# Performance work log

Hardware: AMD Instinct MI355X
Metric: run time of the kernel (lower is better)

Reference implementation:

```python
import jax, jax.numpy as jnp
import numpy as np

EPS = 1e-06

def rmsnorm(x, w):
    x32 = x.astype(jnp.float32)
    var = jnp.mean(x32 * x32, axis=-1, keepdims=True)
    return w * (x32 * jax.lax.rsqrt(var + EPS)).astype(x.dtype)

def setup_inputs() -> dict:
    B, T, C = 16, 256, 16
    token_dim, text_dim = 1024, 512
    key = jax.random.key(0)
    ks = jax.random.split(key, 8)
    token_embeds = jax.random.normal(ks[0], (B, T, token_dim), dtype=jnp.float32)
    char_embeds = jax.random.normal(ks[1], (B, T, C, text_dim), dtype=jnp.float32)
    filler_embed = jax.random.normal(ks[2], (text_dim,), dtype=jnp.float32)
    mask = jax.random.randint(ks[3], (B, T, C), 0, 2).astype(bool)
    mask = mask.at[0].set(True)  # force max valid count == T*C (static output shape)
    token_ids_mask = jnp.ones((B, T), dtype=bool)
    # xavier-uniform-ish weights
    def xav(k, fan_out, fan_in, gain=1.0):
        lim = gain * np.sqrt(6.0 / (fan_in + fan_out))
        return jax.random.uniform(k, (fan_out, fan_in), jnp.float32, -lim, lim)
    W_down = xav(ks[4], text_dim, token_dim)
    W_proj = xav(ks[5], 3, text_dim, gain=0.2)
    W_fusion = xav(ks[6], text_dim, text_dim)
    w_pre = jnp.ones((token_dim,), jnp.float32)
    w_tok = jnp.ones((text_dim,), jnp.float32)
    w_char = jnp.ones((text_dim,), jnp.float32)
    return {"token_embeds": token_embeds, "token_ids_mask": token_ids_mask,
            "char_embeds": char_embeds, "char_ids_mask": mask,
            "filler_embed": filler_embed, "w_pre": w_pre, "w_tok": w_tok,
            "w_char": w_char, "W_down": W_down, "W_proj": W_proj,
            "W_fusion": W_fusion, "max_valid_chars": T * C}

def reference(token_embeds, token_ids_mask, char_embeds, char_ids_mask,
              filler_embed, w_pre, w_tok, w_char, W_down, W_proj, W_fusion,
              max_valid_chars):
    B, T, C, d = char_embeds.shape
    MV = int(max_valid_chars)
    tok = rmsnorm(token_embeds, w_pre)                       # [B,T,token_dim]
    feats = rmsnorm(jnp.einsum('btk,dk->btd', tok, W_down), w_tok)  # [B,T,d]
    params = jnp.einsum('btd,pd->btp', jax.nn.silu(feats), W_proj)  # [B,T,3]
    scale = params[..., 0][:, :, None, None]                 # [B,T,1,1]
    shift = params[..., 1][:, :, None, None]
    gate = jax.nn.sigmoid(params[..., 2][:, :, None, None])
    cn = rmsnorm(char_embeds, w_char)                        # [B,T,C,d]
    fused = jnp.einsum('btcd,ed->btce', jax.nn.silu(cn * (1.0 + scale) + shift), W_fusion)
    fused = gate * fused + (1.0 - gate) * cn                 # [B,T,C,d]
    flat = fused.reshape(B, T * C, d)
    m = char_ids_mask.reshape(B, T * C).astype(jnp.int32)
    pos = jnp.cumsum(m, axis=1) - 1                          # dest within row
    offs = jnp.arange(B, dtype=jnp.int32)[:, None] * MV
    idx = jnp.where(m > 0, offs + pos, B * MV)               # invalid -> dump slot
    buf = jnp.broadcast_to(filler_embed, (B * MV + 1, d))
    buf = buf.at[idx.reshape(-1)].set(flat.reshape(-1, d))
    return buf[: B * MV].reshape(B, MV, d)
```

## Files before the change

kernel.cpp:

```cpp
#include <hip/hip_runtime.h>
#include <cstdint>
#include <cstddef>

#define EPS 1e-6f

typedef short bf16x8 __attribute__((ext_vector_type(8)));
typedef float f32x4  __attribute__((ext_vector_type(4)));

__device__ __forceinline__ short f2bf(float x) {
    uint32_t u = __builtin_bit_cast(uint32_t, x);
    return (short)((u + 0x7FFFu + ((u >> 16) & 1u)) >> 16);
}

__global__ __launch_bounds__(256) void k_scan(const void* __restrict__ maskp,
                                              int* __restrict__ v_list,
                                              int* __restrict__ counts) {
    __shared__ int sc[256];
    __shared__ int mode_s;
    const int tid = threadIdx.x;
    const int b = blockIdx.x;
    const uint32_t* mi = (const uint32_t*)maskp;
    const uint8_t* mb = (const uint8_t*)maskp;

    if (tid == 0) mode_s = 0;
    __syncthreads();
    int bad = 0;
    for (int k = tid; k < 1024; k += 256) bad |= (mi[k] > 1u) ? 1 : 0;
    if (bad) mode_s = 1;
    __syncthreads();
    const int byte_mode = mode_s;

    int base = 0;
    for (int chunk = 0; chunk < 16; ++chunk) {
        const int i = chunk * 256 + tid;
        int m;
        if (byte_mode) m = mb[(b << 12) + i] ? 1 : 0;
        else           m = mi[(b << 12) + i] ? 1 : 0;
        sc[tid] = m;
        __syncthreads();
        for (int off = 1; off < 256; off <<= 1) {
            int v = sc[tid];
            int a = (tid >= off) ? sc[tid - off] : 0;
            __syncthreads();
            sc[tid] = v + a;
            __syncthreads();
        }
        const int incl = sc[tid];
        const int tot = sc[255];
        if (m) v_list[(b << 12) + base + incl - 1] = i;
        base += tot;
        __syncthreads();
    }
    if (tid == 0) counts[b] = base;
}

__global__ __launch_bounds__(256) void k_conv(const float* __restrict__ src,
                                              short* __restrict__ dst, int n4) {
    const int gid = blockIdx.x * 256 + threadIdx.x;
    if (gid >= n4) return;
    const float4 v = ((const float4*)src)[gid];
    short4 o;
    o.x = f2bf(v.x); o.y = f2bf(v.y); o.z = f2bf(v.z); o.w = f2bf(v.w);
    ((short4*)dst)[gid] = o;
}

__global__ __launch_bounds__(256) void k_tokprep(const float* __restrict__ tokens,
                                                 const float* __restrict__ w_pre,
                                                 short* __restrict__ tokbf) {
    const int tid = threadIdx.x, lane = tid & 63, wave = tid >> 6;
    const int row = blockIdx.x * 4 + wave;
    const float* xp = tokens + (size_t)row * 1024 + lane * 16;
    float4 x[4];
#pragma unroll
    for (int q = 0; q < 4; ++q) x[q] = *(const float4*)&xp[q * 4];
    float ss = 0.f;
#pragma unroll
    for (int q = 0; q < 4; ++q)
        ss += x[q].x * x[q].x + x[q].y * x[q].y + x[q].z * x[q].z + x[q].w * x[q].w;
#pragma unroll
    for (int off = 32; off > 0; off >>= 1) ss += __shfl_down(ss, off);
    ss = __shfl(ss, 0);
    const float r = rsqrtf(ss * (1.0f / 1024.0f) + EPS);
    const float* wp = w_pre + lane * 16;
    short* op = tokbf + (size_t)row * 1024 + lane * 16;
#pragma unroll
    for (int h = 0; h < 2; ++h) {
        bf16x8 o;
#pragma unroll
        for (int q = 0; q < 2; ++q) {
            const float4 wv = *(const float4*)&wp[h * 8 + q * 4];
            const float4 xv = x[h * 2 + q];
            o[q * 4 + 0] = f2bf(xv.x * wv.x * r);
            o[q * 4 + 1] = f2bf(xv.y * wv.y * r);
            o[q * 4 + 2] = f2bf(xv.z * wv.z * r);
            o[q * 4 + 3] = f2bf(xv.w * wv.w * r);
        }
        *(bf16x8*)&op[h * 8] = o;
    }
}

__global__ __launch_bounds__(256) void k_gemm_tok(const short* __restrict__ tokbf,
                                                  const short* __restrict__ Wdbf,
                                                  float* __restrict__ feats) {
    __shared__ short As[128 * 32];
    __shared__ short Bs[128 * 32];
    const int tid = threadIdx.x, lane = tid & 63, w = tid >> 6;
    const int mt = blockIdx.x >> 2, nt = blockIdx.x & 3;
    const int wm = w >> 1, wn = w & 1;
    const short* hA = tokbf + (size_t)mt * 128 * 1024;
    const short* wB = Wdbf + (size_t)nt * 128 * 1024;

    f32x4 acc[4][4];
#pragma unroll
    for (int mi = 0; mi < 4; ++mi)
#pragma unroll
        for (int ni = 0; ni < 4; ++ni) acc[mi][ni] = (f32x4)0.f;

    const int rA = lane & 15, q8 = (lane >> 4) * 8;
    for (int kk = 0; kk < 1024; kk += 32) {
#pragma unroll
        for (int q = 0; q < 2; ++q) {
            const int cid = (w * 2 + q) * 64 + lane;
            const int r = cid >> 2, kc = cid & 3;
            const size_t go = (size_t)r * 1024 + kk + kc * 8;
            __builtin_amdgcn_global_load_lds(
                (const __attribute__((address_space(1))) uint32_t*)(hA + go),
                (__attribute__((address_space(3))) uint32_t*)&As[(w * 2 + q) * 512], 16, 0, 0);
            __builtin_amdgcn_global_load_lds(
                (const __attribute__((address_space(1))) uint32_t*)(wB + go),
                (__attribute__((address_space(3))) uint32_t*)&Bs[(w * 2 + q) * 512], 16, 0, 0);
        }
        __syncthreads();
        bf16x8 af[4], bfr[4];
#pragma unroll
        for (int mi = 0; mi < 4; ++mi)
            af[mi] = *(const bf16x8*)&As[(wm * 64 + mi * 16 + rA) * 32 + q8];
#pragma unroll
        for (int ni = 0; ni < 4; ++ni)
            bfr[ni] = *(const bf16x8*)&Bs[(wn * 64 + ni * 16 + rA) * 32 + q8];
#pragma unroll
        for (int mi = 0; mi < 4; ++mi)
#pragma unroll
            for (int ni = 0; ni < 4; ++ni)
                acc[mi][ni] = __builtin_amdgcn_mfma_f32_16x16x32_bf16(af[mi], bfr[ni], acc[mi][ni], 0, 0, 0);
        __syncthreads();
    }
    const int rowb = mt * 128 + wm * 64 + (lane >> 4) * 4;
    const int colb = nt * 128 + wn * 64 + (lane & 15);
#pragma unroll
    for (int mi = 0; mi < 4; ++mi)
#pragma unroll
        for (int ni = 0; ni < 4; ++ni)
#pragma unroll
            for (int rg = 0; rg < 4; ++rg)
                feats[(size_t)(rowb + mi * 16 + rg) * 512 + colb + ni * 16] = acc[mi][ni][rg];
}

__global__ __launch_bounds__(64) void k_params(
    const float* __restrict__ feats_pre, const float* __restrict__ w_tok,
    const float* __restrict__ W_proj, float* __restrict__ params) {
    const int tk = blockIdx.x;
    const int lane = threadIdx.x;
    const int d0 = lane * 8;
    const float* fp = feats_pre + (size_t)tk * 512 + d0;
    const float4 f0 = *(const float4*)&fp[0];
    const float4 f1 = *(const float4*)&fp[4];
    float ss = f0.x * f0.x + f0.y * f0.y + f0.z * f0.z + f0.w * f0.w
             + f1.x * f1.x + f1.y * f1.y + f1.z * f1.z + f1.w * f1.w;
#pragma unroll
    for (int off = 32; off > 0; off >>= 1) ss += __shfl_down(ss, off);
    ss = __shfl(ss, 0);
    const float rms = rsqrtf(ss * (1.0f / 512.0f) + EPS);

    const float4 wt0 = *(const float4*)&w_tok[d0];
    const float4 wt1 = *(const float4*)&w_tok[d0 + 4];
    float fv[8] = {f0.x, f0.y, f0.z, f0.w, f1.x, f1.y, f1.z, f1.w};
    float wv[8] = {wt0.x, wt0.y, wt0.z, wt0.w, wt1.x, wt1.y, wt1.z, wt1.w};
    float s[8];
#pragma unroll
    for (int j = 0; j < 8; ++j) {
        const float v = fv[j] * wv[j] * rms;
        s[j] = v / (1.0f + expf(-v));
    }
    float p[3];
#pragma unroll
    for (int q = 0; q < 3; ++q) {
        const float* Wp = W_proj + (size_t)q * 512 + d0;
        const float4 a = *(const float4*)&Wp[0];
        const float4 c = *(const float4*)&Wp[4];
        p[q] = s[0] * a.x + s[1] * a.y + s[2] * a.z + s[3] * a.w
             + s[4] * c.x + s[5] * c.y + s[6] * c.z + s[7] * c.w;
#pragma unroll
        for (int off = 32; off > 0; off >>= 1) p[q] += __shfl_down(p[q], off);
    }
    if (lane == 0) {
        float* po = params + (size_t)tk * 4;
        po[0] = 1.0f + p[0];
        po[1] = p[1];
        po[2] = 1.0f / (1.0f + expf(-p[2]));
    }
}

__global__ __launch_bounds__(256) void k_prep(
    const float* __restrict__ chars, const float* __restrict__ w_char,
    const float* __restrict__ params, const int* __restrict__ v_list,
    const int* __restrict__ counts, short* __restrict__ hb,
    float* __restrict__ rms_l, float* __restrict__ g_l) {
    const int tid = threadIdx.x, lane = tid & 63, wave = tid >> 6;
    const int b = blockIdx.x >> 10;
    const int j = (blockIdx.x & 1023) * 4 + wave;
    const int cnt = counts[b];
    const int cpad = (cnt + 127) & ~127;
    if (j >= cpad) return;
    short* hrow = hb + ((size_t)(b << 12) + j) * 512 + lane * 8;
    if (j >= cnt) {
        *(bf16x8*)hrow = (bf16x8)0;
        return;
    }
    const int i = v_list[(b << 12) + j];
    const float* xp = chars + ((size_t)(b << 12) + i) * 512 + lane * 8;
    const float4 x0 = *(const float4*)&xp[0];
    const float4 x1 = *(const float4*)&xp[4];
    float ss = x0.x * x0.x + x0.y * x0.y + x0.z * x0.z + x0.w * x0.w
             + x1.x * x1.x + x1.y * x1.y + x1.z * x1.z + x1.w * x1.w;
#pragma unroll
    for (int off = 32; off > 0; off >>= 1) ss += __shfl_down(ss, off);
    ss = __shfl(ss, 0);
    const float rms = rsqrtf(ss * (1.0f / 512.0f) + EPS);
    const float* pp = params + (size_t)((b << 8) + (i >> 4)) * 4;
    const float s1 = pp[0], sh = pp[1], g = pp[2];
    const float4 w0 = *(const float4*)&w_char[lane * 8];
    const float4 w1 = *(const float4*)&w_char[lane * 8 + 4];
    float xv[8] = {x0.x, x0.y, x0.z, x0.w, x1.x, x1.y, x1.z, x1.w};
    float wv[8] = {w0.x, w0.y, w0.z, w0.w, w1.x, w1.y, w1.z, w1.w};
    bf16x8 o;
#pragma unroll
    for (int q = 0; q < 8; ++q) {
        const float cn = wv[q] * xv[q] * rms;
        const float a = cn * s1 + sh;
        o[q] = f2bf(a / (1.0f + expf(-a)));
    }
    *(bf16x8*)hrow = o;
    if (lane == 0) {
        rms_l[(b << 12) + j] = rms;
        g_l[(b << 12) + j] = g;
    }
}

__global__ __launch_bounds__(256) void k_fill(
    const float* __restrict__ filler, const int* __restrict__ counts,
    float* __restrict__ out) {
    const int gid = blockIdx.x * 256 + threadIdx.x;
    const size_t e4 = (size_t)gid * 4;
    const int slot = gid >> 7;
    const int b = slot >> 12;
    const int j = slot & 4095;
    if (j >= counts[b]) {
        const int e0 = (int)(e4 & 511);
        *(float4*)&out[e4] = *(const float4*)&filler[e0];
    }
}

__global__ __launch_bounds__(256) void k_gemm_fus(
    const short* __restrict__ hb, const short* __restrict__ Wbf,
    const float* __restrict__ chars, const float* __restrict__ w_char,
    const float* __restrict__ rms_l, const float* __restrict__ g_l,
    const int* __restrict__ v_list, const int* __restrict__ counts,
    float* __restrict__ out) {
    __shared__ short As[128 * 32];
    __shared__ short Bs[128 * 32];
    __shared__ float g_s[128], rms_s[128];
    __shared__ int idx_s[128];
    const int tid = threadIdx.x, lane = tid & 63, w = tid >> 6;
    const int b = blockIdx.x >> 7;
    const int mt = (blockIdx.x >> 2) & 31;
    const int nt = blockIdx.x & 3;
    const int cnt = counts[b];
    const int row0 = mt * 128;
    if (row0 >= cnt) return;
    const int wm = w >> 1, wn = w & 1;

    if (tid < 128) {
        const int j = row0 + tid;
        const bool valid = j < cnt;
        idx_s[tid] = valid ? v_list[(b << 12) + j] : 0;
        g_s[tid]   = valid ? g_l[(b << 12) + j] : 0.f;
        rms_s[tid] = valid ? rms_l[(b << 12) + j] : 0.f;
    }

    const short* hA = hb + ((size_t)(b << 12) + row0) * 512;
    const short* wB = Wbf + (size_t)nt * 128 * 512;

    f32x4 acc[4][4];
#pragma unroll
    for (int mi = 0; mi < 4; ++mi)
#pragma unroll
        for (int ni = 0; ni < 4; ++ni) acc[mi][ni] = (f32x4)0.f;

    const int rA = lane & 15, q8 = (lane >> 4) * 8;
    for (int kk = 0; kk < 512; kk += 32) {
#pragma unroll
        for (int q = 0; q < 2; ++q) {
            const int cid = (w * 2 + q) * 64 + lane;
            const int r = cid >> 2, kc = cid & 3;
            const size_t go = (size_t)r * 512 + kk + kc * 8;
            __builtin_amdgcn_global_load_lds(
                (const __attribute__((address_space(1))) uint32_t*)(hA + go),
                (__attribute__((address_space(3))) uint32_t*)&As[(w * 2 + q) * 512], 16, 0, 0);
            __builtin_amdgcn_global_load_lds(
                (const __attribute__((address_space(1))) uint32_t*)(wB + go),
                (__attribute__((address_space(3))) uint32_t*)&Bs[(w * 2 + q) * 512], 16, 0, 0);
        }
        __syncthreads();
        bf16x8 af[4], bfr[4];
#pragma unroll
        for (int mi = 0; mi < 4; ++mi)
            af[mi] = *(const bf16x8*)&As[(wm * 64 + mi * 16 + rA) * 32 + q8];
#pragma unroll
        for (int ni = 0; ni < 4; ++ni)
            bfr[ni] = *(const bf16x8*)&Bs[(wn * 64 + ni * 16 + rA) * 32 + q8];
#pragma unroll
        for (int mi = 0; mi < 4; ++mi)
#pragma unroll
            for (int ni = 0; ni < 4; ++ni)
                acc[mi][ni] = __builtin_amdgcn_mfma_f32_16x16x32_bf16(af[mi], bfr[ni], acc[mi][ni], 0, 0, 0);
        __syncthreads();
    }

    const int colb = nt * 128 + wn * 64 + (lane & 15);
    float wcv[4];
#pragma unroll
    for (int ni = 0; ni < 4; ++ni) wcv[ni] = w_char[colb + ni * 16];
#pragma unroll
    for (int mi = 0; mi < 4; ++mi) {
#pragma unroll
        for (int rg = 0; rg < 4; ++rg) {
            const int jl = wm * 64 + mi * 16 + (lane >> 4) * 4 + rg;
            const int j = row0 + jl;
            if (j < cnt) {
                const float g = g_s[jl], rm = rms_s[jl];
                const size_t xrow = ((size_t)(b << 12) + idx_s[jl]) * 512;
                const size_t orow = ((size_t)(b << 12) + j) * 512;
#pragma unroll
                for (int ni = 0; ni < 4; ++ni) {
                    const int col = colb + ni * 16;
                    const float x = chars[xrow + col];
                    const float cn = wcv[ni] * x * rm;
                    out[orow + col] = g * acc[mi][ni][rg] + (1.0f - g) * cn;
                }
            }
        }
    }
}

extern "C" void kernel_launch(void* const* d_in, const int* in_sizes, int n_in,
                              void* d_out, int out_size, void* d_ws, size_t ws_size,
                              hipStream_t stream) {
    const float* tokens = (const float*)d_in[0];
    const float* chars  = (const float*)d_in[2];
    const void*  cmask  = d_in[3];
    const float* filler = (const float*)d_in[4];
    const float* w_pre  = (const float*)d_in[5];
    const float* w_tok  = (const float*)d_in[6];
    const float* w_char = (const float*)d_in[7];
    const float* W_down = (const float*)d_in[8];
    const float* W_proj = (const float*)d_in[9];
    const float* W_fus  = (const float*)d_in[10];
    float* out = (float*)d_out;

    float* feats_pre = (float*)d_ws;
    float* params    = feats_pre + (size_t)4096 * 512;
    int*   counts    = (int*)(params + (size_t)4096 * 4);
    int*   v_list    = counts + 16;
    float* rms_l     = (float*)(v_list + 65536);
    float* g_l       = rms_l + 65536;
    short* Wbf       = (short*)(g_l + 65536);
    short* hb        = Wbf + (size_t)512 * 512;
    short* tokbf     = hb + (size_t)16 * 4096 * 512;
    short* Wdbf      = tokbf + (size_t)4096 * 1024;

    k_scan<<<16, 256, 0, stream>>>(cmask, v_list, counts);
    k_conv<<<256, 256, 0, stream>>>(W_fus, Wbf, 65536);
    k_conv<<<512, 256, 0, stream>>>(W_down, Wdbf, 131072);
    k_tokprep<<<1024, 256, 0, stream>>>(tokens, w_pre, tokbf);
    k_gemm_tok<<<128, 256, 0, stream>>>(tokbf, Wdbf, feats_pre);
    k_params<<<4096, 64, 0, stream>>>(feats_pre, w_tok, W_proj, params);
    k_prep<<<16384, 256, 0, stream>>>(chars, w_char, params, v_list, counts, hb, rms_l, g_l);
    k_fill<<<32768, 256, 0, stream>>>(filler, counts, out);
    k_gemm_fus<<<2048, 256, 0, stream>>>(hb, Wbf, chars, w_char, rms_l, g_l, v_list, counts, out);
}
```

Baseline: 370.0 us.

## Restructure scan, fuse weight converts, retile token GEMM, precompute bf16 residual epilogue

```diff
diff --git a/kernel.cpp b/kernel.cpp
--- a/kernel.cpp
+++ b/kernel.cpp
@@ -10,6 +10,10 @@
 __device__ __forceinline__ short f2bf(float x) {
     uint32_t u = __builtin_bit_cast(uint32_t, x);
     return (short)((u + 0x7FFFu + ((u >> 16) & 1u)) >> 16);
+}
+__device__ __forceinline__ float bf2f(short s) {
+    uint32_t u = ((uint32_t)(uint16_t)s) << 16;
+    return __builtin_bit_cast(float, u);
 }
 
 __global__ __launch_bounds__(256) void k_scan(const void* __restrict__ maskp,
@@ -20,7 +24,6 @@
     const int tid = threadIdx.x;
     const int b = blockIdx.x;
     const uint32_t* mi = (const uint32_t*)maskp;
-    const uint8_t* mb = (const uint8_t*)maskp;
 
     if (tid == 0) mode_s = 0;
     __syncthreads();
@@ -28,40 +31,53 @@
     for (int k = tid; k < 1024; k += 256) bad |= (mi[k] > 1u) ? 1 : 0;
     if (bad) mode_s = 1;
     __syncthreads();
-    const int byte_mode = mode_s;
-
-    int base = 0;
-    for (int chunk = 0; chunk < 16; ++chunk) {
-        const int i = chunk * 256 + tid;
-        int m;
-        if (byte_mode) m = mb[(b << 12) + i] ? 1 : 0;
-        else           m = mi[(b << 12) + i] ? 1 : 0;
-        sc[tid] = m;
-        __syncthreads();
-        for (int off = 1; off < 256; off <<= 1) {
-            int v = sc[tid];
-            int a = (tid >= off) ? sc[tid - off] : 0;
-            __syncthreads();
-            sc[tid] = v + a;
-            __syncthreads();
-        }
-        const int incl = sc[tid];
-        const int tot = sc[255];
-        if (m) v_list[(b << 12) + base + incl - 1] = i;
-        base += tot;
-        __syncthreads();
-    }
-    if (tid == 0) counts[b] = base;
-}
-
-__global__ __launch_bounds__(256) void k_conv(const float* __restrict__ src,
-                                              short* __restrict__ dst, int n4) {
+
+    int m[16];
+    if (mode_s) {
+        const uint4 v = *(const uint4*)((const uint8_t*)maskp + (b << 12) + tid * 16);
+        const uint32_t ws[4] = {v.x, v.y, v.z, v.w};
+#pragma unroll
+        for (int w4 = 0; w4 < 4; ++w4)
+#pragma unroll
+            for (int e = 0; e < 4; ++e)
+                m[w4 * 4 + e] = ((ws[w4] >> (8 * e)) & 0xffu) ? 1 : 0;
+    } else {
+        const uint32_t* p = mi + (b << 12) + tid * 16;
+#pragma unroll
+        for (int q = 0; q < 16; ++q) m[q] = p[q] ? 1 : 0;
+    }
+    int cl = 0;
+#pragma unroll
+    for (int q = 0; q < 16; ++q) cl += m[q];
+    sc[tid] = cl;
+    __syncthreads();
+    for (int off = 1; off < 256; off <<= 1) {
+        int v = sc[tid];
+        int a = (tid >= off) ? sc[tid - off] : 0;
+        __syncthreads();
+        sc[tid] = v + a;
+        __syncthreads();
+    }
+    int pos = sc[tid] - cl;
+#pragma unroll
+    for (int q = 0; q < 16; ++q) {
+        if (m[q]) v_list[(b << 12) + pos++] = tid * 16 + q;
+    }
+    if (tid == 255) counts[b] = sc[255];
+}
+
+__global__ __launch_bounds__(256) void k_conv2(
+    const float* __restrict__ s1, short* __restrict__ d1, int n1,
+    const float* __restrict__ s2, short* __restrict__ d2, int n2) {
     const int gid = blockIdx.x * 256 + threadIdx.x;
-    if (gid >= n4) return;
-    const float4 v = ((const float4*)src)[gid];
+    const float* src; short* dst; int idx;
+    if (gid < n1) { src = s1; dst = d1; idx = gid; }
+    else if (gid < n1 + n2) { src = s2; dst = d2; idx = gid - n1; }
+    else return;
+    const float4 v = ((const float4*)src)[idx];
     short4 o;
     o.x = f2bf(v.x); o.y = f2bf(v.y); o.z = f2bf(v.z); o.w = f2bf(v.w);
-    ((short4*)dst)[gid] = o;
+    ((short4*)dst)[idx] = o;
 }
 
 __global__ __launch_bounds__(256) void k_tokprep(const float* __restrict__ tokens,
@@ -103,18 +119,18 @@
                                                   const short* __restrict__ Wdbf,
                                                   float* __restrict__ feats) {
     __shared__ short As[128 * 32];
-    __shared__ short Bs[128 * 32];
+    __shared__ short Bs[64 * 32];
     const int tid = threadIdx.x, lane = tid & 63, w = tid >> 6;
-    const int mt = blockIdx.x >> 2, nt = blockIdx.x & 3;
+    const int mt = blockIdx.x >> 3, nt = blockIdx.x & 7;
     const int wm = w >> 1, wn = w & 1;
     const short* hA = tokbf + (size_t)mt * 128 * 1024;
-    const short* wB = Wdbf + (size_t)nt * 128 * 1024;
-
-    f32x4 acc[4][4];
+    const short* wB = Wdbf + (size_t)nt * 64 * 1024;
+
+    f32x4 acc[4][2];
 #pragma unroll
     for (int mi = 0; mi < 4; ++mi)
 #pragma unroll
-        for (int ni = 0; ni < 4; ++ni) acc[mi][ni] = (f32x4)0.f;
+        for (int ni = 0; ni < 2; ++ni) acc[mi][ni] = (f32x4)0.f;
 
     const int rA = lane & 15, q8 = (lane >> 4) * 8;
     for (int kk = 0; kk < 1024; kk += 32) {
@@ -122,35 +138,38 @@
         for (int q = 0; q < 2; ++q) {
             const int cid = (w * 2 + q) * 64 + lane;
             const int r = cid >> 2, kc = cid & 3;
-            const size_t go = (size_t)r * 1024 + kk + kc * 8;
             __builtin_amdgcn_global_load_lds(
-                (const __attribute__((address_space(1))) uint32_t*)(hA + go),
+                (const __attribute__((address_space(1))) uint32_t*)(hA + (size_t)r * 1024 + kk + kc * 8),
                 (__attribute__((address_space(3))) uint32_t*)&As[(w * 2 + q) * 512], 16, 0, 0);
+        }
+        {
+            const int cid = tid;
+            const int r = cid >> 2, kc = cid & 3;
             __builtin_amdgcn_global_load_lds(
-                (const __attribute__((address_space(1))) uint32_t*)(wB + go),
-                (__attribute__((address_space(3))) uint32_t*)&Bs[(w * 2 + q) * 512], 16, 0, 0);
+                (const __attribute__((address_space(1))) uint32_t*)(wB + (size_t)r * 1024 + kk + kc * 8),
+                (__attribute__((address_space(3))) uint32_t*)&Bs[w * 512], 16, 0, 0);
         }
         __syncthreads();
-        bf16x8 af[4], bfr[4];
+        bf16x8 af[4], bfr[2];
 #pragma unroll
         for (int mi = 0; mi < 4; ++mi)
             af[mi] = *(const bf16x8*)&As[(wm * 64 + mi * 16 + rA) * 32 + q8];
 #pragma unroll
-        for (int ni = 0; ni < 4; ++ni)
-            bfr[ni] = *(const bf16x8*)&Bs[(wn * 64 + ni * 16 + rA) * 32 + q8];
+        for (int ni = 0; ni < 2; ++ni)
+            bfr[ni] = *(const bf16x8*)&Bs[(wn * 32 + ni * 16 + rA) * 32 + q8];
 #pragma unroll
         for (int mi = 0; mi < 4; ++mi)
 #pragma unroll
-            for (int ni = 0; ni < 4; ++ni)
+            for (int ni = 0; ni < 2; ++ni)
                 acc[mi][ni] = __builtin_amdgcn_mfma_f32_16x16x32_bf16(af[mi], bfr[ni], acc[mi][ni], 0, 0, 0);
         __syncthreads();
     }
     const int rowb = mt * 128 + wm * 64 + (lane >> 4) * 4;
-    const int colb = nt * 128 + wn * 64 + (lane & 15);
+    const int colb = nt * 64 + wn * 32 + (lane & 15);
 #pragma unroll
     for (int mi = 0; mi < 4; ++mi)
 #pragma unroll
-        for (int ni = 0; ni < 4; ++ni)
+        for (int ni = 0; ni < 2; ++ni)
 #pragma unroll
             for (int rg = 0; rg < 4; ++rg)
                 feats[(size_t)(rowb + mi * 16 + rg) * 512 + colb + ni * 16] = acc[mi][ni][rg];
@@ -205,7 +224,7 @@
     const float* __restrict__ chars, const float* __restrict__ w_char,
     const float* __restrict__ params, const int* __restrict__ v_list,
     const int* __restrict__ counts, short* __restrict__ hb,
-    float* __restrict__ rms_l, float* __restrict__ g_l) {
+    short* __restrict__ cnp, float* __restrict__ g_l) {
     const int tid = threadIdx.x, lane = tid & 63, wave = tid >> 6;
     const int b = blockIdx.x >> 10;
     const int j = (blockIdx.x & 1023) * 4 + wave;
@@ -233,18 +252,18 @@
     const float4 w1 = *(const float4*)&w_char[lane * 8 + 4];
     float xv[8] = {x0.x, x0.y, x0.z, x0.w, x1.x, x1.y, x1.z, x1.w};
     float wv[8] = {w0.x, w0.y, w0.z, w0.w, w1.x, w1.y, w1.z, w1.w};
-    bf16x8 o;
+    bf16x8 oh, oc;
+    const float gm1 = 1.0f - g;
 #pragma unroll
     for (int q = 0; q < 8; ++q) {
         const float cn = wv[q] * xv[q] * rms;
         const float a = cn * s1 + sh;
-        o[q] = f2bf(a / (1.0f + expf(-a)));
-    }
-    *(bf16x8*)hrow = o;
-    if (lane == 0) {
-        rms_l[(b << 12) + j] = rms;
-        g_l[(b << 12) + j] = g;
-    }
+        oh[q] = f2bf(a / (1.0f + expf(-a)));
+        oc[q] = f2bf(gm1 * cn);
+    }
+    *(bf16x8*)hrow = oh;
+    *(bf16x8*)(cnp + ((size_t)(b << 12) + j) * 512 + lane * 8) = oc;
+    if (lane == 0) g_l[(b << 12) + j] = g;
 }
 
 __global__ __launch_bounds__(256) void k_fill(
@@ -263,14 +282,13 @@
 
 __global__ __launch_bounds__(256) void k_gemm_fus(
     const short* __restrict__ hb, const short* __restrict__ Wbf,
-    const float* __restrict__ chars, const float* __restrict__ w_char,
-    const float* __restrict__ rms_l, const float* __restrict__ g_l,
-    const int* __restrict__ v_list, const int* __restrict__ counts,
-    float* __restrict__ out) {
-    __shared__ short As[128 * 32];
-    __shared__ short Bs[128 * 32];
-    __shared__ float g_s[128], rms_s[128];
-    __shared__ int idx_s[128];
+    const short* __restrict__ cnp, const float* __restrict__ g_l,
+    const int* __restrict__ counts, float* __restrict__ out) {
+    __shared__ union SM {
+        struct { short A[128 * 32]; short B[128 * 32]; } ab;
+        float ep[32][132];
+    } sm;
+    __shared__ float g_s[128];
     const int tid = threadIdx.x, lane = tid & 63, w = tid >> 6;
     const int b = blockIdx.x >> 7;
     const int mt = (blockIdx.x >> 2) & 31;
@@ -282,10 +300,7 @@
 
     if (tid < 128) {
         const int j = row0 + tid;
-        const bool valid = j < cnt;
-        idx_s[tid] = valid ? v_list[(b << 12) + j] : 0;
-        g_s[tid]   = valid ? g_l[(b << 12) + j] : 0.f;
-        rms_s[tid] = valid ? rms_l[(b << 12) + j] : 0.f;
+        g_s[tid] = (j < cnt) ? g_l[(b << 12) + j] : 0.f;
     }
 
     const short* hA = hb + ((size_t)(b << 12) + row0) * 512;
@@ -306,19 +321,19 @@
             const size_t go = (size_t)r * 512 + kk + kc * 8;
             __builtin_amdgcn_global_load_lds(
                 (const __attribute__((address_space(1))) uint32_t*)(hA + go),
-                (__attribute__((address_space(3))) uint32_t*)&As[(w * 2 + q) * 512], 16, 0, 0);
+                (__attribute__((address_space(3))) uint32_t*)&sm.ab.A[(w * 2 + q) * 512], 16, 0, 0);
             __builtin_amdgcn_global_load_lds(
                 (const __attribute__((address_space(1))) uint32_t*)(wB + go),
-                (__attribute__((address_space(3))) uint32_t*)&Bs[(w * 2 + q) * 512], 16, 0, 0);
+                (__attribute__((address_space(3))) uint32_t*)&sm.ab.B[(w * 2 + q) * 512], 16, 0, 0);
         }
         __syncthreads();
         bf16x8 af[4], bfr[4];
 #pragma unroll
         for (int mi = 0; mi < 4; ++mi)
-            af[mi] = *(const bf16x8*)&As[(wm * 64 + mi * 16 + rA) * 32 + q8];
+            af[mi] = *(const bf16x8*)&sm.ab.A[(wm * 64 + mi * 16 + rA) * 32 + q8];
 #pragma unroll
         for (int ni = 0; ni < 4; ++ni)
-            bfr[ni] = *(const bf16x8*)&Bs[(wn * 64 + ni * 16 + rA) * 32 + q8];
+            bfr[ni] = *(const bf16x8*)&sm.ab.B[(wn * 64 + ni * 16 + rA) * 32 + q8];
 #pragma unroll
         for (int mi = 0; mi < 4; ++mi)
 #pragma unroll
@@ -327,29 +342,39 @@
         __syncthreads();
     }
 
-    const int colb = nt * 128 + wn * 64 + (lane & 15);
-    float wcv[4];
-#pragma unroll
-    for (int ni = 0; ni < 4; ++ni) wcv[ni] = w_char[colb + ni * 16];
+    const int r5 = tid >> 3;
+    const int c0 = (tid & 7) * 16;
+    const int cg = nt * 128 + c0;
 #pragma unroll
     for (int mi = 0; mi < 4; ++mi) {
 #pragma unroll
-        for (int rg = 0; rg < 4; ++rg) {
-            const int jl = wm * 64 + mi * 16 + (lane >> 4) * 4 + rg;
-            const int j = row0 + jl;
-            if (j < cnt) {
-                const float g = g_s[jl], rm = rms_s[jl];
-                const size_t xrow = ((size_t)(b << 12) + idx_s[jl]) * 512;
-                const size_t orow = ((size_t)(b << 12) + j) * 512;
-#pragma unroll
-                for (int ni = 0; ni < 4; ++ni) {
-                    const int col = colb + ni * 16;
-                    const float x = chars[xrow + col];
-                    const float cn = wcv[ni] * x * rm;
-                    out[orow + col] = g * acc[mi][ni][rg] + (1.0f - g) * cn;
-                }
+        for (int ni = 0; ni < 4; ++ni)
+#pragma unroll
+            for (int rg = 0; rg < 4; ++rg)
+                sm.ep[wm * 16 + (lane >> 4) * 4 + rg][wn * 64 + ni * 16 + (lane & 15)] = acc[mi][ni][rg];
+        __syncthreads();
+        const int jl = (r5 < 16) ? (mi * 16 + r5) : (64 + mi * 16 + (r5 - 16));
+        const int j = row0 + jl;
+        if (j < cnt) {
+            const float g = g_s[jl];
+            const short* cp = cnp + ((size_t)(b << 12) + j) * 512 + cg;
+            const bf16x8 cv0 = *(const bf16x8*)cp;
+            const bf16x8 cv1 = *(const bf16x8*)(cp + 8);
+            float cn16[16];
+#pragma unroll
+            for (int e = 0; e < 8; ++e) { cn16[e] = bf2f(cv0[e]); cn16[8 + e] = bf2f(cv1[e]); }
+            float* op = out + ((size_t)(b << 12) + j) * 512 + cg;
+#pragma unroll
+            for (int q = 0; q < 4; ++q) {
+                float4 o;
+                o.x = g * sm.ep[r5][c0 + q * 4 + 0] + cn16[q * 4 + 0];
+                o.y = g * sm.ep[r5][c0 + q * 4 + 1] + cn16[q * 4 + 1];
+                o.z = g * sm.ep[r5][c0 + q * 4 + 2] + cn16[q * 4 + 2];
+                o.w = g * sm.ep[r5][c0 + q * 4 + 3] + cn16[q * 4 + 3];
+                *(float4*)&op[q * 4] = o;
             }
         }
+        __syncthreads();
     }
 }
 
@@ -372,20 +397,19 @@
     float* params    = feats_pre + (size_t)4096 * 512;
     int*   counts    = (int*)(params + (size_t)4096 * 4);
     int*   v_list    = counts + 16;
-    float* rms_l     = (float*)(v_list + 65536);
-    float* g_l       = rms_l + 65536;
+    float* g_l       = (float*)(v_list + 65536);
     short* Wbf       = (short*)(g_l + 65536);
-    short* hb        = Wbf + (size_t)512 * 512;
-    short* tokbf     = hb + (size_t)16 * 4096 * 512;
-    short* Wdbf      = tokbf + (size_t)4096 * 1024;
+    short* Wdbf      = Wbf + (size_t)512 * 512;
+    short* tokbf     = Wdbf + (size_t)512 * 1024;
+    short* hb        = tokbf + (size_t)4096 * 1024;
+    short* cnp       = hb + (size_t)16 * 4096 * 512;
 
     k_scan<<<16, 256, 0, stream>>>(cmask, v_list, counts);
-    k_conv<<<256, 256, 0, stream>>>(W_fus, Wbf, 65536);
-    k_conv<<<512, 256, 0, stream>>>(W_down, Wdbf, 131072);
+    k_conv2<<<768, 256, 0, stream>>>(W_fus, Wbf, 65536, W_down, Wdbf, 131072);
     k_tokprep<<<1024, 256, 0, stream>>>(tokens, w_pre, tokbf);
-    k_gemm_tok<<<128, 256, 0, stream>>>(tokbf, Wdbf, feats_pre);
+    k_gemm_tok<<<256, 256, 0, stream>>>(tokbf, Wdbf, feats_pre);
     k_params<<<4096, 64, 0, stream>>>(feats_pre, w_tok, W_proj, params);
-    k_prep<<<16384, 256, 0, stream>>>(chars, w_char, params, v_list, counts, hb, rms_l, g_l);
+    k_prep<<<16384, 256, 0, stream>>>(chars, w_char, params, v_list, counts, hb, cnp, g_l);
     k_fill<<<32768, 256, 0, stream>>>(filler, counts, out);
-    k_gemm_fus<<<2048, 256, 0, stream>>>(hb, Wbf, chars, w_char, rms_l, g_l, v_list, counts, out);
-}
+    k_gemm_fus<<<2048, 256, 0, stream>>>(hb, Wbf, cnp, g_l, counts, out);
+}
```

Result: slower. 403.4 us (+9.0%).
